# Performance work log

Measured on AMD Instinct MI355X. Metric: run time of the kernel, lower is better.

## Reference

```python
import jax, jax.numpy as jnp
import numpy as np

T, L, N, DR = 8, 8, 500, 32
D = 2 * DR          # dr2 = 64
K = 12              # neighbors per region
S = 2               # number_sp attention layers


def setup_inputs() -> dict:
    key = jax.random.key(0)
    ks = jax.random.split(key, 14)
    inp = {}
    inp["all_data_static"] = jax.random.normal(ks[0], (T, L, N, D), jnp.float32)
    inp["thre_nc"] = jax.random.uniform(ks[1], (T, L, N, 1), jnp.float32)
    inp["all_data_dynamic_now"] = jax.random.uniform(ks[2], (L, N, D), jnp.float32)
    inp["neigh_poi"] = jax.random.randint(ks[3], (N, K), 0, N)
    inp["neigh_road"] = jax.random.randint(ks[4], (N, K), 0, N)
    inp["neigh_record"] = jax.random.randint(ks[5], (N, K), 0, N)
    inp["w1"] = jax.random.normal(ks[6], (2 * D, D), jnp.float32) * 0.05
    inp["wq_all"] = jax.random.normal(ks[7], (2, 3, S, D, D), jnp.float32) * 0.05
    inp["wk_all"] = jax.random.normal(ks[8], (2, 3, S, D, D), jnp.float32) * 0.05
    inp["wd_all"] = jax.random.normal(ks[9], (2, 3, S, D, D), jnp.float32) * 0.05
    inp["wmix_all"] = jax.random.normal(ks[10], (2, 3, D), jnp.float32) * 0.1
    inp["conv_w"] = jax.random.normal(ks[11], (4, 2 * D + 1), jnp.float32) * 0.05
    inp["conv_b"] = jnp.zeros((4,), jnp.float32)
    inp["fin_w"] = jax.random.normal(ks[12], (N, N), jnp.float32) * 0.02
    inp["fin_b"] = jnp.ones((N,), jnp.float32)
    return inp


def _attention(data, neigh, wq, wk, wd):
    # data: (T,L,N,D), neigh: (N,K)
    dn = data[:, :, neigh, :]                                   # (T,L,N,K,D) gather
    q = jnp.einsum('tlnd,de->tlne', data, wq)                   # (T,L,N,D)
    k = jnp.einsum('tlnkd,de->tlnke', dn, wk)                   # (T,L,N,K,D)
    a = jax.nn.softmax(jnp.einsum('tlne,tlnke->tlnk', q, k), -1)
    out = q + jnp.einsum('tlnk,tlnke->tlne', a, k)              # residual on q
    return jax.nn.sigmoid(jnp.einsum('tlnd,de->tlne', out, wd))


def _multiattention(data, neighs, wq, wk, wd, wmix):
    outs = []
    for g in range(3):  # poi, road, record
        x = data
        for s in range(wq.shape[1]):
            x = _attention(x, neighs[g], wq[g, s], wk[g, s], wd[g, s])
        outs.append(x)
    return jax.nn.sigmoid(outs[0] * wmix[0] + outs[1] * wmix[1] + outs[2] * wmix[2])


def reference(all_data_static, thre_nc, all_data_dynamic_now,
              neigh_poi, neigh_road, neigh_record,
              w1, wq_all, wk_all, wd_all, wmix_all,
              conv_w, conv_b, fin_w, fin_b):
    # --- Evolution: gated recurrence over time steps 1..T-1 ---
    def evo_step(now, xs):
        st, th = xs  # (L,N,D), (L,N,1)
        new = jax.nn.sigmoid(jnp.concatenate([now, st], -1) @ w1 * th
                             + now * (1.0 - th))
        return new, (new, new - now)
    now_final, (dyn_rest, diffs) = jax.lax.scan(
        evo_step, all_data_dynamic_now, (all_data_static[1:], thre_nc[1:]))
    all_dyn = jnp.concatenate([all_data_dynamic_now[None], dyn_rest], 0)  # (T,L,N,D)

    neighs = (neigh_poi, neigh_road, neigh_record)
    dyn = _multiattention(all_dyn, neighs, wq_all[0], wk_all[0], wd_all[0], wmix_all[0])
    sta = _multiattention(all_data_static, neighs, wq_all[1], wk_all[1], wd_all[1], wmix_all[1])
    x = jnp.concatenate([dyn, sta], -1)                          # (T,L,N,2D)

    # --- ConvLSTM, kernel (1,1), hidden_dim=1 -> pointwise gated recurrence ---
    h0 = jnp.zeros((x.shape[0], x.shape[2], 1), x.dtype)         # (T,N,1)
    def cell(carry, xt):  # xt: (T,N,2D)
        h, c = carry
        gates = jnp.concatenate([xt, h], -1) @ conv_w.T + conv_b  # (T,N,4)
        i = jax.nn.sigmoid(gates[..., 0:1])
        f = jax.nn.sigmoid(gates[..., 1:2])
        o = jax.nn.sigmoid(gates[..., 2:3])
        g = jnp.tanh(gates[..., 3:4])
        c2 = f * c + i * g
        h2 = o * jnp.tanh(c2)
        return (h2, c2), None
    (h_last, _), _ = jax.lax.scan(cell, (h0, h0), jnp.swapaxes(x, 0, 1))

    out = jax.nn.sigmoid(h_last[..., 0] @ fin_w.T + fin_b)       # (T,N)
    return out, now_final, diffs
```

## Files before the change

### kernel.cpp

```cpp
#include <hip/hip_runtime.h>
#include <math.h>

namespace {
constexpr int kT = 8, kL = 8, kN = 500, kD = 64, kK = 12;
constexpr int kLN  = kL * kN;
constexpr int kTLN = kT * kL * kN;
constexpr int kBUF = kTLN * kD;
constexpr int XS = 68;
}

__device__ __forceinline__ float sigf(float v) { return 1.f / (1.f + __expf(-v)); }

__device__ __forceinline__ uint2 pack_bf16x4(float4 v) {
    auto r = [](float f) {
        unsigned u = __float_as_uint(f);
        u += 0x7FFFu + ((u >> 16) & 1u);
        return u >> 16;
    };
    uint2 o;
    o.x = r(v.x) | (r(v.y) << 16);
    o.y = r(v.z) | (r(v.w) << 16);
    return o;
}

__device__ __forceinline__ float4 unpack_bf16x4(uint2 kk) {
    float4 f;
    f.x = __uint_as_float(kk.x << 16);
    f.y = __uint_as_float(kk.x & 0xFFFF0000u);
    f.z = __uint_as_float(kk.y << 16);
    f.w = __uint_as_float(kk.y & 0xFFFF0000u);
    return f;
}

__device__ __forceinline__ void stage_x_wave(const float* __restrict__ src, float* lds,
                                             int row0, int M) {
    int lane = threadIdx.x & 63, w = threadIdx.x >> 6;
    int rr = 16 * w + (lane >> 2);
    int row = row0 + rr;
    row = row < M ? row : M - 1;
    int f0 = lane & 3;
#pragma unroll
    for (int i = 0; i < 4; ++i) {
        int f = f0 + 4 * i;
        float4 v = *reinterpret_cast<const float4*>(src + (size_t)row * 64 + f * 4);
        *reinterpret_cast<float4*>(lds + rr * XS + f * 4) = v;
    }
}

__device__ __forceinline__ void stage_x_bf16_wave(const unsigned short* __restrict__ src,
                                                  float* lds, int row0) {
    int lane = threadIdx.x & 63, w = threadIdx.x >> 6;
    int rr = 16 * w + (lane >> 2);
    int f0 = lane & 3;
#pragma unroll
    for (int i = 0; i < 4; ++i) {
        int f = f0 + 4 * i;
        uint2 v = *reinterpret_cast<const uint2*>(src + (size_t)(row0 + rr) * 64 + f * 4);
        *reinterpret_cast<float4*>(lds + rr * XS + f * 4) = unpack_bf16x4(v);
    }
}

template <int K>
__device__ __forceinline__ void stage_w(const float* __restrict__ w, float* lds) {
    const float4* s = reinterpret_cast<const float4*>(w);
    float4* d = reinterpret_cast<float4*>(lds);
#pragma unroll
    for (int i = 0; i < K / 16; ++i)
        d[threadIdx.x + 256 * i] = s[threadIdx.x + 256 * i];
}

__device__ __forceinline__ void gemm_core(const float* ldsx, const float* w,
                                          int rblk, int cblk, float4 acc[4]) {
#pragma unroll 4
    for (int k = 0; k < 64; k += 4) {
        float4 xv[4], wv[4];
#pragma unroll
        for (int i = 0; i < 4; ++i)
            xv[i] = *reinterpret_cast<const float4*>(ldsx + (4 * rblk + i) * XS + k);
#pragma unroll
        for (int d = 0; d < 4; ++d)
            wv[d] = *reinterpret_cast<const float4*>(w + (k + d) * 64 + 4 * cblk);
#pragma unroll
        for (int i = 0; i < 4; ++i) {
            float xs[4] = {xv[i].x, xv[i].y, xv[i].z, xv[i].w};
#pragma unroll
            for (int d = 0; d < 4; ++d) {
                acc[i].x = fmaf(xs[d], wv[d].x, acc[i].x);
                acc[i].y = fmaf(xs[d], wv[d].y, acc[i].y);
                acc[i].z = fmaf(xs[d], wv[d].z, acc[i].z);
                acc[i].w = fmaf(xs[d], wv[d].w, acc[i].w);
            }
        }
    }
}

__device__ __forceinline__ void gemm_core2(const float* ldsx, const float* wa,
                                           const float* wb, int rblk, int cblk,
                                           float4 acca[4], float4 accb[4]) {
#pragma unroll 4
    for (int k = 0; k < 64; k += 4) {
        float4 xv[4], va[4], vb[4];
#pragma unroll
        for (int i = 0; i < 4; ++i)
            xv[i] = *reinterpret_cast<const float4*>(ldsx + (4 * rblk + i) * XS + k);
#pragma unroll
        for (int d = 0; d < 4; ++d) {
            va[d] = *reinterpret_cast<const float4*>(wa + (k + d) * 64 + 4 * cblk);
            vb[d] = *reinterpret_cast<const float4*>(wb + (k + d) * 64 + 4 * cblk);
        }
#pragma unroll
        for (int i = 0; i < 4; ++i) {
            float xs[4] = {xv[i].x, xv[i].y, xv[i].z, xv[i].w};
#pragma unroll
            for (int d = 0; d < 4; ++d) {
                acca[i].x = fmaf(xs[d], va[d].x, acca[i].x);
                acca[i].y = fmaf(xs[d], va[d].y, acca[i].y);
                acca[i].z = fmaf(xs[d], va[d].z, acca[i].z);
                acca[i].w = fmaf(xs[d], va[d].w, acca[i].w);
                accb[i].x = fmaf(xs[d], vb[d].x, accb[i].x);
                accb[i].y = fmaf(xs[d], vb[d].y, accb[i].y);
                accb[i].z = fmaf(xs[d], vb[d].z, accb[i].z);
                accb[i].w = fmaf(xs[d], vb[d].w, accb[i].w);
            }
        }
    }
}

__device__ __forceinline__ void score_phase(const uint2* __restrict__ Qb,
                                            const uint2* __restrict__ Kb,
                                            const int* __restrict__ neigh,
                                            float* ldsx, int row0) {
    int lane = threadIdx.x & 63;
    int w    = threadIdx.x >> 6;
    int sub  = lane >> 4;
    int gq   = lane & 15;
#pragma unroll 1
    for (int pp = 0; pp < 4; ++pp) {
        int lr  = 16 * w + 4 * pp + sub;
        int row = row0 + lr;
        int n   = row % kN;
        int slab = row - n;
        float4 q = unpack_bf16x4(Qb[(size_t)row * 16 + gq]);
        const int4* nbp = reinterpret_cast<const int4*>(neigh + n * kK);
        int4 nb0 = nbp[0], nb1 = nbp[1], nb2 = nbp[2];
        int nb[12] = {nb0.x, nb0.y, nb0.z, nb0.w, nb1.x, nb1.y, nb1.z, nb1.w,
                      nb2.x, nb2.y, nb2.z, nb2.w};
        float4 kv[12];
        float sc[12];
#pragma unroll
        for (int j = 0; j < 12; ++j) {
            kv[j] = unpack_bf16x4(Kb[(size_t)(slab + nb[j]) * 16 + gq]);
            sc[j] = q.x * kv[j].x + q.y * kv[j].y + q.z * kv[j].z + q.w * kv[j].w;
        }
#pragma unroll
        for (int off = 1; off < 16; off <<= 1) {
#pragma unroll
            for (int j = 0; j < 12; ++j) sc[j] += __shfl_xor(sc[j], off, 16);
        }
        float mx = sc[0];
#pragma unroll
        for (int j = 1; j < 12; ++j) mx = fmaxf(mx, sc[j]);
        float ssum = 0.f;
#pragma unroll
        for (int j = 0; j < 12; ++j) { sc[j] = __expf(sc[j] - mx); ssum += sc[j]; }
        float inv = 1.f / ssum;
        float4 o = q;
#pragma unroll
        for (int j = 0; j < 12; ++j) {
            float a = sc[j] * inv;
            o.x = fmaf(a, kv[j].x, o.x);
            o.y = fmaf(a, kv[j].y, o.y);
            o.z = fmaf(a, kv[j].z, o.z);
            o.w = fmaf(a, kv[j].w, o.w);
        }
        *reinterpret_cast<float4*>(ldsx + lr * XS + 4 * gq) = o;
    }
}

__global__ void __launch_bounds__(256) evo_all_kernel(const float* __restrict__ stat,
                                                      const float* __restrict__ thre,
                                                      const float* __restrict__ dyn0,
                                                      float* __restrict__ all_dyn,
                                                      float* __restrict__ diff,
                                                      float* __restrict__ now_final,
                                                      const float* __restrict__ w1) {
    __shared__ float ldsn[64 * XS];
    __shared__ float ldss[64 * XS];
    __shared__ float ldsw[128 * 64];
    int row0 = blockIdx.x * 64;
    stage_x_wave(dyn0, ldsn, row0, kLN);
    stage_w<128>(w1, ldsw);
    int rblk = threadIdx.x >> 4, cblk = threadIdx.x & 15;
    __syncthreads();
#pragma unroll
    for (int i = 0; i < 4; ++i) {
        int row = row0 + 4 * rblk + i;
        if (row < kLN) {
            float4 x0 = *reinterpret_cast<const float4*>(ldsn + (4 * rblk + i) * XS + 4 * cblk);
            *reinterpret_cast<float4*>(all_dyn + (size_t)row * 64 + 4 * cblk) = x0;
        }
    }
#pragma unroll 1
    for (int t = 1; t < kT; ++t) {
        stage_x_wave(stat + (size_t)t * kLN * kD, ldss, row0, kLN);
        float4 acc[4] = {};
        gemm_core(ldsn, ldsw, rblk, cblk, acc);
        gemm_core(ldss, ldsw + 64 * 64, rblk, cblk, acc);
        float4 nv[4];
#pragma unroll
        for (int i = 0; i < 4; ++i) {
            int row = row0 + 4 * rblk + i;
            int rc  = row < kLN ? row : kLN - 1;
            float tt = thre[t * kLN + rc];
            float4 xn = *reinterpret_cast<const float4*>(ldsn + (4 * rblk + i) * XS + 4 * cblk);
            nv[i].x = sigf(acc[i].x * tt + xn.x * (1.f - tt));
            nv[i].y = sigf(acc[i].y * tt + xn.y * (1.f - tt));
            nv[i].z = sigf(acc[i].z * tt + xn.z * (1.f - tt));
            nv[i].w = sigf(acc[i].w * tt + xn.w * (1.f - tt));
            if (row < kLN) {
                float4 df;
                df.x = nv[i].x - xn.x; df.y = nv[i].y - xn.y;
                df.z = nv[i].z - xn.z; df.w = nv[i].w - xn.w;
                *reinterpret_cast<float4*>(all_dyn + ((size_t)t * kLN + row) * 64 + 4 * cblk) = nv[i];
                *reinterpret_cast<float4*>(diff + ((size_t)(t - 1) * kLN + row) * 64 + 4 * cblk) = df;
                if (t == kT - 1)
                    *reinterpret_cast<float4*>(now_final + (size_t)row * 64 + 4 * cblk) = nv[i];
            }
        }
#pragma unroll
        for (int i = 0; i < 4; ++i)
            *reinterpret_cast<float4*>(ldsn + (4 * rblk + i) * XS + 4 * cblk) = nv[i];
    }
}

__global__ void __launch_bounds__(256) gemm_qk(const float* __restrict__ Xdyn,
                                               const float* __restrict__ Xstat,
                                               const float* __restrict__ wq_all,
                                               const float* __restrict__ wk_all,
                                               unsigned short* __restrict__ b1,
                                               unsigned short* __restrict__ b2,
                                               int step) {
    __shared__ float ldsx[64 * XS];
    int c = blockIdx.y;
    int m = c / 3;
    unsigned short* b1c = b1 + (size_t)c * kBUF;
    unsigned short* kc  = b2 + (size_t)c * kBUF;
    const float* gwq = wq_all + (size_t)(c * 2 + step) * kD * kD;
    const float* gwk = wk_all + (size_t)(c * 2 + step) * kD * kD;
    int row0 = blockIdx.x * 64;
    if (step) stage_x_bf16_wave(b1c, ldsx, row0);
    else      stage_x_wave(m == 0 ? Xdyn : Xstat, ldsx, row0, kTLN);
    int rblk = threadIdx.x >> 4, cblk = threadIdx.x & 15;
    float4 aq[4] = {}, ak[4] = {};
    gemm_core2(ldsx, gwq, gwk, rblk, cblk, aq, ak);
#pragma unroll
    for (int i = 0; i < 4; ++i) {
        size_t row = row0 + 4 * rblk + i;
        *reinterpret_cast<uint2*>(b1c + row * 64 + 4 * cblk) = pack_bf16x4(aq[i]);
        *reinterpret_cast<uint2*>(kc + row * 64 + 4 * cblk)  = pack_bf16x4(ak[i]);
    }
}

__global__ void __launch_bounds__(256) scorewd_kernel(unsigned short* __restrict__ b1,
                                                      const unsigned short* __restrict__ b2,
                                                      const int* __restrict__ npoi,
                                                      const int* __restrict__ nroad,
                                                      const int* __restrict__ nrec,
                                                      const float* __restrict__ wd_all,
                                                      int step) {
    __shared__ float ldsx[64 * XS];
    int p   = blockIdx.y * gridDim.x + blockIdx.x;
    int xcd = p & 7;
    int gid = xcd * 375 + (p >> 3);
    int c    = gid / 500;
    int tile = gid - c * 500;
    int g = c % 3;
    unsigned short* b1c = b1 + (size_t)c * kBUF;
    const uint2* Qb = reinterpret_cast<const uint2*>(b1c);
    const uint2* Kb = reinterpret_cast<const uint2*>(b2 + (size_t)c * kBUF);
    const int* neigh = (g == 0) ? npoi : (g == 1) ? nroad : nrec;
    const float* gwd = wd_all + (size_t)(c * 2 + step) * kD * kD;
    int row0 = tile * 64;

    score_phase(Qb, Kb, neigh, ldsx, row0);

    int rblk = threadIdx.x >> 4, cblk = threadIdx.x & 15;
    float4 acc[4] = {};
    gemm_core(ldsx, gwd, rblk, cblk, acc);
#pragma unroll
    for (int i = 0; i < 4; ++i) {
        size_t row = row0 + 4 * rblk + i;
        float4 y;
        y.x = sigf(acc[i].x); y.y = sigf(acc[i].y);
        y.z = sigf(acc[i].z); y.w = sigf(acc[i].w);
        *reinterpret_cast<uint2*>(b1c + row * 64 + 4 * cblk) = pack_bf16x4(y);
    }
}

__global__ void __launch_bounds__(256) lstm_kernel(const unsigned short* __restrict__ b1,
                                                   const float* __restrict__ wmix,
                                                   const float* __restrict__ cw,
                                                   const float* __restrict__ cb,
                                                   float* __restrict__ hlast) {
    int lane = threadIdx.x & 63;
    int wv   = threadIdx.x >> 6;
    int sub  = lane >> 4;
    int fq   = lane & 15;
    int cell = blockIdx.x * 16 + wv * 4 + sub;
    int t = cell / kN, n = cell % kN;
    float wd_[4][4], ws_[4][4], wh[4], bb[4];
#pragma unroll
    for (int gg = 0; gg < 4; ++gg) {
#pragma unroll
        for (int k = 0; k < 4; ++k) {
            wd_[gg][k] = cw[gg * 129 + fq * 4 + k];
            ws_[gg][k] = cw[gg * 129 + 64 + fq * 4 + k];
        }
        wh[gg] = cw[gg * 129 + 128];
        bb[gg] = cb[gg];
    }
    float4 wm[6];
#pragma unroll
    for (int j = 0; j < 6; ++j)
        wm[j] = *reinterpret_cast<const float4*>(wmix + j * 64 + fq * 4);
    float h = 0.f, cc = 0.f;
#pragma unroll 1
    for (int l = 0; l < kL; ++l) {
        size_t base = ((size_t)(t * kL + l) * kN + n) * 64 + fq * 4;
        float4 y[6];
#pragma unroll
        for (int j = 0; j < 6; ++j)
            y[j] = unpack_bf16x4(*reinterpret_cast<const uint2*>(b1 + (size_t)j * kBUF + base));
        float4 xd, xs;
        xd.x = sigf(y[0].x * wm[0].x + y[1].x * wm[1].x + y[2].x * wm[2].x);
        xd.y = sigf(y[0].y * wm[0].y + y[1].y * wm[1].y + y[2].y * wm[2].y);
        xd.z = sigf(y[0].z * wm[0].z + y[1].z * wm[1].z + y[2].z * wm[2].z);
        xd.w = sigf(y[0].w * wm[0].w + y[1].w * wm[1].w + y[2].w * wm[2].w);
        xs.x = sigf(y[3].x * wm[3].x + y[4].x * wm[4].x + y[5].x * wm[5].x);
        xs.y = sigf(y[3].y * wm[3].y + y[4].y * wm[4].y + y[5].y * wm[5].y);
        xs.z = sigf(y[3].z * wm[3].z + y[4].z * wm[4].z + y[5].z * wm[5].z);
        xs.w = sigf(y[3].w * wm[3].w + y[4].w * wm[4].w + y[5].w * wm[5].w);
        float gsum[4];
#pragma unroll
        for (int gg = 0; gg < 4; ++gg) {
            float v = xd.x * wd_[gg][0] + xd.y * wd_[gg][1]
                    + xd.z * wd_[gg][2] + xd.w * wd_[gg][3];
            v += xs.x * ws_[gg][0] + xs.y * ws_[gg][1]
               + xs.z * ws_[gg][2] + xs.w * ws_[gg][3];
            gsum[gg] = v;
        }
#pragma unroll
        for (int off = 1; off < 16; off <<= 1) {
#pragma unroll
            for (int gg = 0; gg < 4; ++gg) gsum[gg] += __shfl_xor(gsum[gg], off, 16);
        }
        float gi = sigf(gsum[0] + bb[0] + h * wh[0]);
        float gf = sigf(gsum[1] + bb[1] + h * wh[1]);
        float go = sigf(gsum[2] + bb[2] + h * wh[2]);
        float gg_ = tanhf(gsum[3] + bb[3] + h * wh[3]);
        cc = gf * cc + gi * gg_;
        h = go * tanhf(cc);
    }
    if (fq == 0) hlast[cell] = h;
}

__global__ void final_kernel(const float* __restrict__ h, const float* __restrict__ fw,
                             const float* __restrict__ fb, float* __restrict__ out) {
    int wave = threadIdx.x >> 6, lane = threadIdx.x & 63;
    int o = blockIdx.x * 4 + wave;
    int t = o / kN, m = o % kN;
    float acc = 0.f;
    for (int n = lane; n < kN; n += 64)
        acc = fmaf(h[t * kN + n], fw[(size_t)m * kN + n], acc);
#pragma unroll
    for (int off = 32; off > 0; off >>= 1) acc += __shfl_xor(acc, off);
    if (lane == 0) out[o] = sigf(acc + fb[m]);
}

extern "C" void kernel_launch(void* const* d_in, const int* in_sizes, int n_in,
                              void* d_out, int out_size, void* d_ws, size_t ws_size,
                              hipStream_t stream) {
    const float* stat   = (const float*)d_in[0];
    const float* thre   = (const float*)d_in[1];
    const float* dyn0   = (const float*)d_in[2];
    const int*   npoi   = (const int*)d_in[3];
    const int*   nroad  = (const int*)d_in[4];
    const int*   nrec   = (const int*)d_in[5];
    const float* w1     = (const float*)d_in[6];
    const float* wq_all = (const float*)d_in[7];
    const float* wk_all = (const float*)d_in[8];
    const float* wd_all = (const float*)d_in[9];
    const float* wmix   = (const float*)d_in[10];
    const float* conv_w = (const float*)d_in[11];
    const float* conv_b = (const float*)d_in[12];
    const float* fin_w  = (const float*)d_in[13];
    const float* fin_b  = (const float*)d_in[14];

    float* out       = (float*)d_out;
    float* now_final = out + kT * kN;
    float* diffs     = now_final + (size_t)kLN * kD;

    float* ws      = (float*)d_ws;
    float* all_dyn = ws;
    unsigned short* b1 = (unsigned short*)(ws + (size_t)kBUF);
    unsigned short* b2 = (unsigned short*)(ws + 4 * (size_t)kBUF);
    float* hlast   = ws + 7 * (size_t)kBUF;

    evo_all_kernel<<<(kLN + 63) / 64, 256, 0, stream>>>(stat, thre, dyn0,
                                                        all_dyn, diffs, now_final, w1);

    dim3 agrid(kTLN / 64, 6);
    gemm_qk<<<agrid, 256, 0, stream>>>(all_dyn, stat, wq_all, wk_all, b1, b2, 0);
    scorewd_kernel<<<agrid, 256, 0, stream>>>(b1, b2, npoi, nroad, nrec, wd_all, 0);
    gemm_qk<<<agrid, 256, 0, stream>>>(all_dyn, stat, wq_all, wk_all, b1, b2, 1);
    scorewd_kernel<<<agrid, 256, 0, stream>>>(b1, b2, npoi, nroad, nrec, wd_all, 1);

    lstm_kernel<<<kT * kN / 16, 256, 0, stream>>>(b1, wmix, conv_w, conv_b, hlast);
    final_kernel<<<kT * kN / 4, 256, 0, stream>>>(hlast, fin_w, fin_b, out);
}
```

Baseline: 367.1 us.

## Fold attention weights into precomputed products so scoring skips the per-row Wd GEMM

Precomputes Wq·Wkᵀ, Wq·Wd and Wk·Wd per layer inside the first kernel's spare blocks. The projection kernel now emits P = X·WqWkᵀ, QD = X·WqWd and KD = X·WkWd. The score kernel computes scores as P·x_neighbor and sigmoid(QD + Σ a·KD_neighbor), so the second per-row 64x64 GEMM after attention is removed. This trades that GEMM for a third projection output, an extra gathered neighbor read of raw X alongside KD, more bf16 buffers, and a different rounding path.

```diff
diff --git a/kernel.cpp b/kernel.cpp
--- a/kernel.cpp
+++ b/kernel.cpp
@@ -94,12 +94,13 @@
     }
 }
 
-__device__ __forceinline__ void gemm_core2(const float* ldsx, const float* wa,
-                                           const float* wb, int rblk, int cblk,
-                                           float4 acca[4], float4 accb[4]) {
-#pragma unroll 4
+__device__ __forceinline__ void gemm_core3(const float* ldsx, const float* wa,
+                                           const float* wb, const float* wc,
+                                           int rblk, int cblk,
+                                           float4 aa[4], float4 ab[4], float4 ac[4]) {
+#pragma unroll 2
     for (int k = 0; k < 64; k += 4) {
-        float4 xv[4], va[4], vb[4];
+        float4 xv[4], va[4], vb[4], vc[4];
 #pragma unroll
         for (int i = 0; i < 4; ++i)
             xv[i] = *reinterpret_cast<const float4*>(ldsx + (4 * rblk + i) * XS + k);
@@ -107,86 +108,113 @@
         for (int d = 0; d < 4; ++d) {
             va[d] = *reinterpret_cast<const float4*>(wa + (k + d) * 64 + 4 * cblk);
             vb[d] = *reinterpret_cast<const float4*>(wb + (k + d) * 64 + 4 * cblk);
+            vc[d] = *reinterpret_cast<const float4*>(wc + (k + d) * 64 + 4 * cblk);
         }
 #pragma unroll
         for (int i = 0; i < 4; ++i) {
             float xs[4] = {xv[i].x, xv[i].y, xv[i].z, xv[i].w};
 #pragma unroll
             for (int d = 0; d < 4; ++d) {
-                acca[i].x = fmaf(xs[d], va[d].x, acca[i].x);
-                acca[i].y = fmaf(xs[d], va[d].y, acca[i].y);
-                acca[i].z = fmaf(xs[d], va[d].z, acca[i].z);
-                acca[i].w = fmaf(xs[d], va[d].w, acca[i].w);
-                accb[i].x = fmaf(xs[d], vb[d].x, accb[i].x);
-                accb[i].y = fmaf(xs[d], vb[d].y, accb[i].y);
-                accb[i].z = fmaf(xs[d], vb[d].z, accb[i].z);
-                accb[i].w = fmaf(xs[d], vb[d].w, accb[i].w);
+                aa[i].x = fmaf(xs[d], va[d].x, aa[i].x);
+                aa[i].y = fmaf(xs[d], va[d].y, aa[i].y);
+                aa[i].z = fmaf(xs[d], va[d].z, aa[i].z);
+                aa[i].w = fmaf(xs[d], va[d].w, aa[i].w);
+                ab[i].x = fmaf(xs[d], vb[d].x, ab[i].x);
+                ab[i].y = fmaf(xs[d], vb[d].y, ab[i].y);
+                ab[i].z = fmaf(xs[d], vb[d].z, ab[i].z);
+                ab[i].w = fmaf(xs[d], vb[d].w, ab[i].w);
+                ac[i].x = fmaf(xs[d], vc[d].x, ac[i].x);
+                ac[i].y = fmaf(xs[d], vc[d].y, ac[i].y);
+                ac[i].z = fmaf(xs[d], vc[d].z, ac[i].z);
+                ac[i].w = fmaf(xs[d], vc[d].w, ac[i].w);
             }
         }
     }
 }
 
-__device__ __forceinline__ void score_phase(const uint2* __restrict__ Qb,
-                                            const uint2* __restrict__ Kb,
-                                            const int* __restrict__ neigh,
-                                            float* ldsx, int row0) {
-    int lane = threadIdx.x & 63;
-    int w    = threadIdx.x >> 6;
-    int sub  = lane >> 4;
-    int gq   = lane & 15;
-#pragma unroll 1
-    for (int pp = 0; pp < 4; ++pp) {
-        int lr  = 16 * w + 4 * pp + sub;
-        int row = row0 + lr;
-        int n   = row % kN;
-        int slab = row - n;
-        float4 q = unpack_bf16x4(Qb[(size_t)row * 16 + gq]);
-        const int4* nbp = reinterpret_cast<const int4*>(neigh + n * kK);
-        int4 nb0 = nbp[0], nb1 = nbp[1], nb2 = nbp[2];
-        int nb[12] = {nb0.x, nb0.y, nb0.z, nb0.w, nb1.x, nb1.y, nb1.z, nb1.w,
-                      nb2.x, nb2.y, nb2.z, nb2.w};
-        float4 kv[12];
-        float sc[12];
-#pragma unroll
-        for (int j = 0; j < 12; ++j) {
-            kv[j] = unpack_bf16x4(Kb[(size_t)(slab + nb[j]) * 16 + gq]);
-            sc[j] = q.x * kv[j].x + q.y * kv[j].y + q.z * kv[j].z + q.w * kv[j].w;
-        }
-#pragma unroll
-        for (int off = 1; off < 16; off <<= 1) {
-#pragma unroll
-            for (int j = 0; j < 12; ++j) sc[j] += __shfl_xor(sc[j], off, 16);
-        }
-        float mx = sc[0];
-#pragma unroll
-        for (int j = 1; j < 12; ++j) mx = fmaxf(mx, sc[j]);
-        float ssum = 0.f;
-#pragma unroll
-        for (int j = 0; j < 12; ++j) { sc[j] = __expf(sc[j] - mx); ssum += sc[j]; }
-        float inv = 1.f / ssum;
-        float4 o = q;
-#pragma unroll
-        for (int j = 0; j < 12; ++j) {
-            float a = sc[j] * inv;
-            o.x = fmaf(a, kv[j].x, o.x);
-            o.y = fmaf(a, kv[j].y, o.y);
-            o.z = fmaf(a, kv[j].z, o.z);
-            o.w = fmaf(a, kv[j].w, o.w);
-        }
-        *reinterpret_cast<float4*>(ldsx + lr * XS + 4 * gq) = o;
-    }
-}
-
-__global__ void __launch_bounds__(256) evo_all_kernel(const float* __restrict__ stat,
-                                                      const float* __restrict__ thre,
-                                                      const float* __restrict__ dyn0,
-                                                      float* __restrict__ all_dyn,
-                                                      float* __restrict__ diff,
-                                                      float* __restrict__ now_final,
-                                                      const float* __restrict__ w1) {
+__device__ __forceinline__ void small_gemm_nn(const float* __restrict__ A,
+                                              const float* __restrict__ B,
+                                              float* __restrict__ Out) {
+    int rblk = threadIdx.x >> 4, cblk = threadIdx.x & 15;
+    float4 acc[4] = {};
+#pragma unroll 4
+    for (int k = 0; k < 64; k += 4) {
+        float4 a[4], b[4];
+#pragma unroll
+        for (int i = 0; i < 4; ++i)
+            a[i] = *reinterpret_cast<const float4*>(A + (4 * rblk + i) * 64 + k);
+#pragma unroll
+        for (int d = 0; d < 4; ++d)
+            b[d] = *reinterpret_cast<const float4*>(B + (k + d) * 64 + 4 * cblk);
+#pragma unroll
+        for (int i = 0; i < 4; ++i) {
+            float xs[4] = {a[i].x, a[i].y, a[i].z, a[i].w};
+#pragma unroll
+            for (int d = 0; d < 4; ++d) {
+                acc[i].x = fmaf(xs[d], b[d].x, acc[i].x);
+                acc[i].y = fmaf(xs[d], b[d].y, acc[i].y);
+                acc[i].z = fmaf(xs[d], b[d].z, acc[i].z);
+                acc[i].w = fmaf(xs[d], b[d].w, acc[i].w);
+            }
+        }
+    }
+#pragma unroll
+    for (int i = 0; i < 4; ++i)
+        *reinterpret_cast<float4*>(Out + (4 * rblk + i) * 64 + 4 * cblk) = acc[i];
+}
+
+__device__ __forceinline__ void small_gemm_nt(const float* __restrict__ A,
+                                              const float* __restrict__ B,
+                                              float* __restrict__ Out) {
+    int rblk = threadIdx.x >> 4, cblk = threadIdx.x & 15;
+    float4 acc[4] = {};
+#pragma unroll 4
+    for (int k = 0; k < 64; k += 4) {
+        float4 a[4], b[4];
+#pragma unroll
+        for (int i = 0; i < 4; ++i)
+            a[i] = *reinterpret_cast<const float4*>(A + (4 * rblk + i) * 64 + k);
+#pragma unroll
+        for (int j = 0; j < 4; ++j)
+            b[j] = *reinterpret_cast<const float4*>(B + (4 * cblk + j) * 64 + k);
+#pragma unroll
+        for (int i = 0; i < 4; ++i) {
+            acc[i].x += a[i].x * b[0].x + a[i].y * b[0].y + a[i].z * b[0].z + a[i].w * b[0].w;
+            acc[i].y += a[i].x * b[1].x + a[i].y * b[1].y + a[i].z * b[1].z + a[i].w * b[1].w;
+            acc[i].z += a[i].x * b[2].x + a[i].y * b[2].y + a[i].z * b[2].z + a[i].w * b[2].w;
+            acc[i].w += a[i].x * b[3].x + a[i].y * b[3].y + a[i].z * b[3].z + a[i].w * b[3].w;
+        }
+    }
+#pragma unroll
+    for (int i = 0; i < 4; ++i)
+        *reinterpret_cast<float4*>(Out + (4 * rblk + i) * 64 + 4 * cblk) = acc[i];
+}
+
+__global__ void __launch_bounds__(256) evo_wprep_kernel(const float* __restrict__ stat,
+                                                        const float* __restrict__ thre,
+                                                        const float* __restrict__ dyn0,
+                                                        float* __restrict__ all_dyn,
+                                                        float* __restrict__ diff,
+                                                        float* __restrict__ now_final,
+                                                        const float* __restrict__ w1,
+                                                        const float* __restrict__ wq_all,
+                                                        const float* __restrict__ wk_all,
+                                                        const float* __restrict__ wd_all,
+                                                        float* __restrict__ wpM,
+                                                        float* __restrict__ wpQ,
+                                                        float* __restrict__ wpK) {
     __shared__ float ldsn[64 * XS];
     __shared__ float ldss[64 * XS];
     __shared__ float ldsw[128 * 64];
+    if (blockIdx.x >= 63) {
+        int i = blockIdx.x - 63;
+        int kind = i % 3;
+        size_t cs = (size_t)(i / 3) * kD * kD;
+        if (kind == 0)      small_gemm_nt(wq_all + cs, wk_all + cs, wpM + cs);
+        else if (kind == 1) small_gemm_nn(wq_all + cs, wd_all + cs, wpQ + cs);
+        else                small_gemm_nn(wk_all + cs, wd_all + cs, wpK + cs);
+        return;
+    }
     int row0 = blockIdx.x * 64;
     stage_x_wave(dyn0, ldsn, row0, kLN);
     stage_w<128>(w1, ldsw);
@@ -233,67 +261,120 @@
     }
 }
 
-__global__ void __launch_bounds__(256) gemm_qk(const float* __restrict__ Xdyn,
-                                               const float* __restrict__ Xstat,
-                                               const float* __restrict__ wq_all,
-                                               const float* __restrict__ wk_all,
-                                               unsigned short* __restrict__ b1,
-                                               unsigned short* __restrict__ b2,
-                                               int step) {
+__global__ void __launch_bounds__(256) proj_kernel(const float* __restrict__ Xdyn,
+                                                   const float* __restrict__ Xstat,
+                                                   const unsigned short* __restrict__ b_y,
+                                                   const float* __restrict__ wpM,
+                                                   const float* __restrict__ wpQ,
+                                                   const float* __restrict__ wpK,
+                                                   unsigned short* __restrict__ b_p,
+                                                   unsigned short* __restrict__ b_qd,
+                                                   unsigned short* __restrict__ b_kd,
+                                                   int step) {
     __shared__ float ldsx[64 * XS];
     int c = blockIdx.y;
     int m = c / 3;
-    unsigned short* b1c = b1 + (size_t)c * kBUF;
-    unsigned short* kc  = b2 + (size_t)c * kBUF;
-    const float* gwq = wq_all + (size_t)(c * 2 + step) * kD * kD;
-    const float* gwk = wk_all + (size_t)(c * 2 + step) * kD * kD;
+    size_t cs = (size_t)(c * 2 + step) * kD * kD;
     int row0 = blockIdx.x * 64;
-    if (step) stage_x_bf16_wave(b1c, ldsx, row0);
+    if (step) stage_x_bf16_wave(b_y + (size_t)c * kBUF, ldsx, row0);
     else      stage_x_wave(m == 0 ? Xdyn : Xstat, ldsx, row0, kTLN);
     int rblk = threadIdx.x >> 4, cblk = threadIdx.x & 15;
-    float4 aq[4] = {}, ak[4] = {};
-    gemm_core2(ldsx, gwq, gwk, rblk, cblk, aq, ak);
+    float4 aP[4] = {}, aQ[4] = {}, aK[4] = {};
+    gemm_core3(ldsx, wpM + cs, wpQ + cs, wpK + cs, rblk, cblk, aP, aQ, aK);
+    unsigned short* pc  = b_p  + (size_t)c * kBUF;
+    unsigned short* qc  = b_qd + (size_t)c * kBUF;
+    unsigned short* kc  = b_kd + (size_t)c * kBUF;
 #pragma unroll
     for (int i = 0; i < 4; ++i) {
         size_t row = row0 + 4 * rblk + i;
-        *reinterpret_cast<uint2*>(b1c + row * 64 + 4 * cblk) = pack_bf16x4(aq[i]);
-        *reinterpret_cast<uint2*>(kc + row * 64 + 4 * cblk)  = pack_bf16x4(ak[i]);
-    }
-}
-
-__global__ void __launch_bounds__(256) scorewd_kernel(unsigned short* __restrict__ b1,
-                                                      const unsigned short* __restrict__ b2,
-                                                      const int* __restrict__ npoi,
-                                                      const int* __restrict__ nroad,
-                                                      const int* __restrict__ nrec,
-                                                      const float* __restrict__ wd_all,
-                                                      int step) {
-    __shared__ float ldsx[64 * XS];
+        *reinterpret_cast<uint2*>(pc + row * 64 + 4 * cblk) = pack_bf16x4(aP[i]);
+        *reinterpret_cast<uint2*>(qc + row * 64 + 4 * cblk) = pack_bf16x4(aQ[i]);
+        *reinterpret_cast<uint2*>(kc + row * 64 + 4 * cblk) = pack_bf16x4(aK[i]);
+    }
+}
+
+__global__ void __launch_bounds__(256) score_kernel(const unsigned short* __restrict__ b_p,
+                                                    const unsigned short* __restrict__ b_qd,
+                                                    const unsigned short* __restrict__ b_kd,
+                                                    const float* __restrict__ Xdyn,
+                                                    const float* __restrict__ Xstat,
+                                                    const unsigned short* __restrict__ b_y_in,
+                                                    unsigned short* __restrict__ Ybase,
+                                                    const int* __restrict__ npoi,
+                                                    const int* __restrict__ nroad,
+                                                    const int* __restrict__ nrec,
+                                                    int step) {
     int p   = blockIdx.y * gridDim.x + blockIdx.x;
     int xcd = p & 7;
     int gid = xcd * 375 + (p >> 3);
     int c    = gid / 500;
     int tile = gid - c * 500;
-    int g = c % 3;
-    unsigned short* b1c = b1 + (size_t)c * kBUF;
-    const uint2* Qb = reinterpret_cast<const uint2*>(b1c);
-    const uint2* Kb = reinterpret_cast<const uint2*>(b2 + (size_t)c * kBUF);
+    int m = c / 3, g = c % 3;
+    const uint2* P  = reinterpret_cast<const uint2*>(b_p  + (size_t)c * kBUF);
+    const uint2* QD = reinterpret_cast<const uint2*>(b_qd + (size_t)c * kBUF);
+    const uint2* KD = reinterpret_cast<const uint2*>(b_kd + (size_t)c * kBUF);
+    const float* Xf = (m == 0) ? Xdyn : Xstat;
+    const uint2* Xb = reinterpret_cast<const uint2*>(b_y_in + (size_t)c * kBUF);
+    unsigned short* Y = Ybase + (size_t)c * kBUF;
     const int* neigh = (g == 0) ? npoi : (g == 1) ? nroad : nrec;
-    const float* gwd = wd_all + (size_t)(c * 2 + step) * kD * kD;
+    int lane = threadIdx.x & 63;
+    int wv   = threadIdx.x >> 6;
+    int sub  = lane >> 4;
+    int gq   = lane & 15;
     int row0 = tile * 64;
-
-    score_phase(Qb, Kb, neigh, ldsx, row0);
-
-    int rblk = threadIdx.x >> 4, cblk = threadIdx.x & 15;
-    float4 acc[4] = {};
-    gemm_core(ldsx, gwd, rblk, cblk, acc);
-#pragma unroll
-    for (int i = 0; i < 4; ++i) {
-        size_t row = row0 + 4 * rblk + i;
+#pragma unroll 1
+    for (int pp = 0; pp < 4; ++pp) {
+        int row = row0 + pp * 16 + wv * 4 + sub;
+        int n   = row % kN;
+        int slab = row - n;
+        const int4* nbp = reinterpret_cast<const int4*>(neigh + n * kK);
+        int4 nb0 = nbp[0], nb1 = nbp[1], nb2 = nbp[2];
+        int nb[12] = {nb0.x, nb0.y, nb0.z, nb0.w, nb1.x, nb1.y, nb1.z, nb1.w,
+                      nb2.x, nb2.y, nb2.z, nb2.w};
+        uint2 kdr[12];
+#pragma unroll
+        for (int j = 0; j < 12; ++j)
+            kdr[j] = KD[(size_t)(slab + nb[j]) * 16 + gq];
+        float4 pv = unpack_bf16x4(P[(size_t)row * 16 + gq]);
+        float sc[12];
+        if (step == 0) {
+#pragma unroll
+            for (int j = 0; j < 12; ++j) {
+                float4 xj = *(reinterpret_cast<const float4*>(Xf) + (size_t)(slab + nb[j]) * 16 + gq);
+                sc[j] = pv.x * xj.x + pv.y * xj.y + pv.z * xj.z + pv.w * xj.w;
+            }
+        } else {
+#pragma unroll
+            for (int j = 0; j < 12; ++j) {
+                float4 xj = unpack_bf16x4(Xb[(size_t)(slab + nb[j]) * 16 + gq]);
+                sc[j] = pv.x * xj.x + pv.y * xj.y + pv.z * xj.z + pv.w * xj.w;
+            }
+        }
+#pragma unroll
+        for (int off = 1; off < 16; off <<= 1) {
+#pragma unroll
+            for (int j = 0; j < 12; ++j) sc[j] += __shfl_xor(sc[j], off, 16);
+        }
+        float mx = sc[0];
+#pragma unroll
+        for (int j = 1; j < 12; ++j) mx = fmaxf(mx, sc[j]);
+        float ssum = 0.f;
+#pragma unroll
+        for (int j = 0; j < 12; ++j) { sc[j] = __expf(sc[j] - mx); ssum += sc[j]; }
+        float inv = 1.f / ssum;
+        float4 o = unpack_bf16x4(QD[(size_t)row * 16 + gq]);
+#pragma unroll
+        for (int j = 0; j < 12; ++j) {
+            float a = sc[j] * inv;
+            float4 kd = unpack_bf16x4(kdr[j]);
+            o.x = fmaf(a, kd.x, o.x);
+            o.y = fmaf(a, kd.y, o.y);
+            o.z = fmaf(a, kd.z, o.z);
+            o.w = fmaf(a, kd.w, o.w);
+        }
         float4 y;
-        y.x = sigf(acc[i].x); y.y = sigf(acc[i].y);
-        y.z = sigf(acc[i].z); y.w = sigf(acc[i].w);
-        *reinterpret_cast<uint2*>(b1c + row * 64 + 4 * cblk) = pack_bf16x4(y);
+        y.x = sigf(o.x); y.y = sigf(o.y); y.z = sigf(o.z); y.w = sigf(o.w);
+        *reinterpret_cast<uint2*>(Y + (size_t)row * 64 + 4 * gq) = pack_bf16x4(y);
     }
 }
 
@@ -402,19 +483,29 @@
 
     float* ws      = (float*)d_ws;
     float* all_dyn = ws;
-    unsigned short* b1 = (unsigned short*)(ws + (size_t)kBUF);
-    unsigned short* b2 = (unsigned short*)(ws + 4 * (size_t)kBUF);
-    float* hlast   = ws + 7 * (size_t)kBUF;
-
-    evo_all_kernel<<<(kLN + 63) / 64, 256, 0, stream>>>(stat, thre, dyn0,
-                                                        all_dyn, diffs, now_final, w1);
+    unsigned short* b_qd = (unsigned short*)(ws + (size_t)kBUF);
+    unsigned short* b_p  = (unsigned short*)(ws + 4 * (size_t)kBUF);
+    unsigned short* b_kd = (unsigned short*)(ws + 7 * (size_t)kBUF);
+    unsigned short* b_y  = (unsigned short*)(ws + 10 * (size_t)kBUF);
+    float* wpM   = ws + 13 * (size_t)kBUF;
+    float* wpQ   = wpM + 12 * 4096;
+    float* wpK   = wpQ + 12 * 4096;
+    float* hlast = wpK + 12 * 4096;
+
+    evo_wprep_kernel<<<63 + 36, 256, 0, stream>>>(stat, thre, dyn0, all_dyn, diffs,
+                                                  now_final, w1, wq_all, wk_all, wd_all,
+                                                  wpM, wpQ, wpK);
 
     dim3 agrid(kTLN / 64, 6);
-    gemm_qk<<<agrid, 256, 0, stream>>>(all_dyn, stat, wq_all, wk_all, b1, b2, 0);
-    scorewd_kernel<<<agrid, 256, 0, stream>>>(b1, b2, npoi, nroad, nrec, wd_all, 0);
-    gemm_qk<<<agrid, 256, 0, stream>>>(all_dyn, stat, wq_all, wk_all, b1, b2, 1);
-    scorewd_kernel<<<agrid, 256, 0, stream>>>(b1, b2, npoi, nroad, nrec, wd_all, 1);
-
-    lstm_kernel<<<kT * kN / 16, 256, 0, stream>>>(b1, wmix, conv_w, conv_b, hlast);
+    proj_kernel<<<agrid, 256, 0, stream>>>(all_dyn, stat, b_y, wpM, wpQ, wpK,
+                                           b_p, b_qd, b_kd, 0);
+    score_kernel<<<agrid, 256, 0, stream>>>(b_p, b_qd, b_kd, all_dyn, stat, b_y,
+                                            b_y, npoi, nroad, nrec, 0);
+    proj_kernel<<<agrid, 256, 0, stream>>>(all_dyn, stat, b_y, wpM, wpQ, wpK,
+                                           b_p, b_qd, b_kd, 1);
+    score_kernel<<<agrid, 256, 0, stream>>>(b_p, b_qd, b_kd, all_dyn, stat, b_y,
+                                            b_qd, npoi, nroad, nrec, 1);
+
+    lstm_kernel<<<kT * kN / 16, 256, 0, stream>>>(b_qd, wmix, conv_w, conv_b, hlast);
     final_kernel<<<kT * kN / 4, 256, 0, stream>>>(hlast, fin_w, fin_b, out);
 }
```

New measurement: 402.1 us. 9.6% more time.
